# Kernel optimization log

Hardware: AMD Instinct MI355X
Metric: run time of the kernel (lower is better)

The kernel has to match this reference:

```python
import jax, jax.numpy as jnp
import numpy as np

BN_EPS = 1e-5
K = 3  # kernel size


def conv2d(x, w, b, pad):
    y = jax.lax.conv_general_dilated(
        x, w, window_strides=(1, 1), padding=[(pad, pad), (pad, pad)],
        dimension_numbers=('NCHW', 'OIHW', 'NCHW'))
    return y + b[None, :, None, None]


def setup_inputs() -> dict:
    key = jax.random.key(0)
    ks = jax.random.split(key, 4)
    B, C, H, W, O = 8, 256, 64, 64, 256
    x = jax.random.normal(ks[0], (B, C, H, W), dtype=jnp.float32)
    # offset/mask conv: 3*dg*k*k = 27 out channels; small init -> small offsets
    w_off = jax.random.normal(ks[1], (27, C, K, K), dtype=jnp.float32) * 0.01
    b_off = jnp.zeros((27,), dtype=jnp.float32)
    # main deformable conv weight/bias
    w = jax.random.normal(ks[2], (O, C, K, K), dtype=jnp.float32) * 0.05
    b = jnp.zeros((O,), dtype=jnp.float32)
    # BatchNorm (inference) params / running stats
    gamma = jnp.ones((O,), dtype=jnp.float32)
    beta = jnp.zeros((O,), dtype=jnp.float32)
    run_mean = jnp.zeros((O,), dtype=jnp.float32)
    run_var = jnp.ones((O,), dtype=jnp.float32)
    return {"x": x, "w_off": w_off, "b_off": b_off, "w": w, "b": b,
            "gamma": gamma, "beta": beta, "run_mean": run_mean, "run_var": run_var}


def _dcn_bn_relu(x, w_off, b_off, w, b, gamma, beta, run_mean, run_var):
    B, C, H, W = x.shape
    KK = K * K
    # offset + modulation mask (DCNv2): channels [0:9]=dy, [9:18]=dx, [18:27]=mask
    om = conv2d(x, w_off, b_off, pad=1)            # [B, 27, H, W]
    dy, dx = om[:, :KK], om[:, KK:2 * KK]          # [B, 9, H, W]
    mod = jax.nn.sigmoid(om[:, 2 * KK:])           # [B, 9, H, W]

    ky, kx = jnp.meshgrid(jnp.arange(K), jnp.arange(K), indexing='ij')
    # base sampling grid: out pixel + dilation*(k - center), padding=1
    base_y = jnp.arange(H, dtype=jnp.float32)[None, :, None] - 1.0 + ky.reshape(KK, 1, 1)
    base_x = jnp.arange(W, dtype=jnp.float32)[None, None, :] - 1.0 + kx.reshape(KK, 1, 1)
    py = base_y[None] + dy                          # [B, 9, H, W]
    px = base_x[None] + dx

    y0 = jnp.floor(py); x0 = jnp.floor(px)
    fy = py - y0; fx = px - x0
    y0 = y0.astype(jnp.int32); x0 = x0.astype(jnp.int32)

    x_flat = x.reshape(B, C, H * W)
    gather = jax.vmap(lambda xf, idx: xf[:, idx])   # ([C,HW],[9,H,W]) -> [C,9,H,W]

    def corner(yi, xi, wgt):
        valid = (yi >= 0) & (yi < H) & (xi >= 0) & (xi < W)
        idx = jnp.clip(yi, 0, H - 1) * W + jnp.clip(xi, 0, W - 1)
        val = gather(x_flat, idx)                   # [B, C, 9, H, W]
        return val * (wgt * valid.astype(wgt.dtype))[:, None]

    sampled = (corner(y0,     x0,     (1 - fy) * (1 - fx))
               + corner(y0,     x0 + 1, (1 - fy) * fx)
               + corner(y0 + 1, x0,     fy * (1 - fx))
               + corner(y0 + 1, x0 + 1, fy * fx))    # [B, C, 9, H, W]
    sampled = sampled * mod[:, None]                 # modulation

    O = w.shape[0]
    out = jnp.einsum('bckhw,ock->bohw', sampled, w.reshape(O, C, KK))
    out = out + b[None, :, None, None]

    # BatchNorm2d (inference) + ReLU
    inv = gamma / jnp.sqrt(run_var + BN_EPS)
    out = out * inv[None, :, None, None] + (beta - run_mean * inv)[None, :, None, None]
    return jax.nn.relu(out)


def reference(x, w_off, b_off, w, b, gamma, beta, run_mean, run_var):
    return _dcn_bn_relu(x, w_off, b_off, w, b, gamma, beta, run_mean, run_var)
```

## Files before the change

### kernel.cpp

```cpp
#include <hip/hip_runtime.h>
#include <math.h>

#define B_   8
#define C_   256
#define H_   64
#define W_   64
#define O_   256
#define KK_  9
#define CK_  2304
#define HW_  4096
#define BN_EPS 1e-5f

typedef __bf16 bf16x8 __attribute__((ext_vector_type(8)));
typedef float  f32x4  __attribute__((ext_vector_type(4)));

static __device__ __forceinline__ unsigned short f2bf(float f) {
    unsigned int u = __float_as_uint(f);
    unsigned int r = (u + 0x7fffu + ((u >> 16) & 1u)) >> 16;
    return (unsigned short)r;
}
static __device__ __forceinline__ unsigned int packbf2(float lo, float hi) {
    unsigned int ul = __float_as_uint(lo) + 0x8000u;
    unsigned int uh = __float_as_uint(hi) + 0x8000u;
    return __builtin_amdgcn_perm(uh, ul, 0x07060302u);
}
static __device__ __forceinline__ float bflo(unsigned int u) {
    return __uint_as_float(u << 16);
}
static __device__ __forceinline__ float bfhi(unsigned int u) {
    return __uint_as_float(u & 0xffff0000u);
}

__global__ __launch_bounds__(256) void prep_kernel(
    const float* __restrict__ x, const float* __restrict__ w,
    const float* __restrict__ w_off,
    unsigned short* __restrict__ xT, unsigned short* __restrict__ wKf,
    unsigned short* __restrict__ wof)
{
    __shared__ float tile[64][65];
    __shared__ float wbuf[4608];

    const int blk = blockIdx.x;
    const int tid = threadIdx.x, lane = tid & 63, tg = tid >> 6;

    if (blk < 512) {
        const int L = (blk & 7) * 64 + (blk >> 3);
        const int b = L & 7, h = L >> 3;
        const int hwb = h * W_;
#pragma unroll
        for (int ct = 0; ct < 4; ++ct) {
            const int c0 = ct * 64;
#pragma unroll
            for (int r = 0; r < 16; ++r) {
                int c_l = tg + r * 4;
                tile[c_l][lane] = x[((size_t)(b * C_ + c0 + c_l)) * HW_ + hwb + lane];
            }
            __syncthreads();
#pragma unroll
            for (int it = 0; it < 4; ++it) {
                const int hw_l = tg * 16 + it * 4 + (lane >> 4);
                const int c_l4 = (lane & 15) * 4;
                float v0 = tile[c_l4 + 0][hw_l];
                float v1 = tile[c_l4 + 1][hw_l];
                float v2 = tile[c_l4 + 2][hw_l];
                float v3 = tile[c_l4 + 3][hw_l];
                uint2 pk;
                pk.x = packbf2(v0, v1);
                pk.y = packbf2(v2, v3);
                *(uint2*)&xT[((size_t)(b * HW_ + hwb + hw_l)) * C_ + c0 + c_l4] = pk;
            }
            __syncthreads();
        }
    } else if (blk < 640) {
        const int t2 = blk - 512;
        const int NT = t2 >> 3, cb = t2 & 7;
#pragma unroll
        for (int i = 0; i < 18; ++i) {
            int j = i * 256 + tid;
            int o_l = j / 288, rest = j - o_l * 288;
            wbuf[o_l * 288 + rest] = w[(size_t)(NT * 16 + o_l) * CK_ + cb * 288 + rest];
        }
        __syncthreads();
#pragma unroll
        for (int i = 0; i < 18; ++i) {
            int d = i * 256 + tid;
            int tap = d >> 9, r5 = d & 511;
            int ln = r5 >> 3, e = r5 & 7;
            int n16 = ln & 15, q = ln >> 4;
            float val = wbuf[n16 * 288 + (q * 8 + e) * 9 + tap];
            wKf[((size_t)(NT * 72 + tap * 8 + cb) * 64 + ln) * 8 + e] = f2bf(val);
        }
    } else {
        const int t2 = blk - 640;
        const int NT = t2 >> 3, cb = t2 & 7;
#pragma unroll
        for (int i = 0; i < 18; ++i) {
            int j = i * 256 + tid;
            int o_l = j / 288, rest = j - o_l * 288;
            int o = NT * 16 + o_l;
            wbuf[o_l * 288 + rest] =
                (o < 27) ? w_off[(size_t)o * CK_ + cb * 288 + rest] : 0.f;
        }
        __syncthreads();
#pragma unroll
        for (int i = 0; i < 18; ++i) {
            int d = i * 256 + tid;
            int tap = d >> 9, r5 = d & 511;
            int ln = r5 >> 3, e = r5 & 7;
            int n16 = ln & 15, q = ln >> 4;
            float val = wbuf[n16 * 288 + (q * 8 + e) * 9 + tap];
            wof[((size_t)(NT * 72 + tap * 8 + cb) * 64 + ln) * 8 + e] = f2bf(val);
        }
    }
}

__global__ __launch_bounds__(512, 4) void dcn_fused_kernel(
    const unsigned short* __restrict__ xT, const unsigned short* __restrict__ wKf,
    const unsigned short* __restrict__ wof, const float* __restrict__ b_off,
    const float* __restrict__ bias, const float* __restrict__ gamma,
    const float* __restrict__ beta, const float* __restrict__ rmean,
    const float* __restrict__ rvar, float* __restrict__ out)
{
    __shared__ __align__(16) unsigned char smem[74528];
    unsigned short* rowbuf = (unsigned short*)smem;
    float4*         wgtv   = (float4*)smem;
    int4*           idxv   = (int4*)(smem + 9216);
    typedef float OmbT[27][64];
    OmbT& omb = *(OmbT*)(smem + 34848);
    typedef unsigned short AbufT[8][4][64][8];
    AbufT& Abuf = *(AbufT*)(smem + 41760);

    const int pblk = blockIdx.x;
    const int L = (pblk & 7) * 64 + (pblk >> 3);
    const int b = L & 7, h = L >> 3;
    const int tid = threadIdx.x, lane = tid & 63, wv = tid >> 6;
    const int m16 = lane & 15, q = lane >> 4;

    if (tid < 33) {
        *(uint4*)&rowbuf[tid * 8] = make_uint4(0u, 0u, 0u, 0u);
    } else if (tid >= 256 && tid < 289) {
        *(uint4*)&rowbuf[65 * 264 + (tid - 256) * 8] = make_uint4(0u, 0u, 0u, 0u);
    }

    const int mi_a = wv & 3, nj_a = wv >> 2;
    f32x4 oacc = {0.f, 0.f, 0.f, 0.f};
    const uint4* wof4 = (const uint4*)wof;

    for (int r = 0; r < 3; ++r) {
        const int hh = h - 1 + r;
        const bool vr = (hh >= 0) && (hh < H_);
        __syncthreads();
        if (vr) {
            const uint4* src = (const uint4*)&xT[((size_t)(b * HW_ + hh * W_)) * C_];
#pragma unroll
            for (int i = 0; i < 4; ++i) {
                const int idx8 = i * 512 + tid;
                uint4 v = src[idx8];
                const int px = idx8 >> 5, c8 = (idx8 & 31) * 8;
                *(uint4*)&rowbuf[(px + 1) * 264 + c8] = v;
            }
        }
        __syncthreads();
        if (vr) {
#pragma unroll
            for (int s = 0; s < 3; ++s) {
                const unsigned short* arow = &rowbuf[(mi_a * 16 + m16 + s) * 264 + q * 8];
#pragma unroll
                for (int cc = 0; cc < 8; ++cc) {
                    bf16x8 a = *(const bf16x8*)&arow[cc * 32];
                    uint4 braw = wof4[(size_t)(nj_a * 72 + (r * 3 + s) * 8 + cc) * 64 + lane];
                    oacc = __builtin_amdgcn_mfma_f32_16x16x32_bf16(
                        a, __builtin_bit_cast(bf16x8, braw), oacc, 0, 0, 0);
                }
            }
        }
    }
    {
        const int t = nj_a * 16 + m16;
        if (t < 27) {
            const float bo = b_off[t];
            float s0 = oacc[0] + bo, s1 = oacc[1] + bo,
                  s2 = oacc[2] + bo, s3 = oacc[3] + bo;
            if (t >= 18) {
                s0 = 1.f / (1.f + expf(-s0));
                s1 = 1.f / (1.f + expf(-s1));
                s2 = 1.f / (1.f + expf(-s2));
                s3 = 1.f / (1.f + expf(-s3));
            }
            float4 rr; rr.x = s0; rr.y = s1; rr.z = s2; rr.w = s3;
            *(float4*)&omb[t][mi_a * 16 + q * 4] = rr;
        }
    }
    __syncthreads();

    for (int i = tid; i < 576; i += 512) {
        int p = i / 9, t = i - p * 9;
        float dy = omb[t][p];
        float dx = omb[t + 9][p];
        float md = omb[t + 18][p];
        float py = (float)(h - 1 + t / 3) + dy;
        float px = (float)(p - 1 + t % 3) + dx;
        float y0f = floorf(py), x0f = floorf(px);
        int   y0 = (int)y0f,    x0 = (int)x0f;
        float fy = py - y0f,    fx = px - x0f;
        int y0c = min(max(y0,     0), H_ - 1), y1c = min(max(y0 + 1, 0), H_ - 1);
        int x0c = min(max(x0,     0), W_ - 1), x1c = min(max(x0 + 1, 0), W_ - 1);
        float vy0 = (y0     >= 0 && y0     < H_) ? 1.f : 0.f;
        float vy1 = (y0 + 1 >= 0 && y0 + 1 < H_) ? 1.f : 0.f;
        float vx0 = (x0     >= 0 && x0     < W_) ? 1.f : 0.f;
        float vx1 = (x0 + 1 >= 0 && x0 + 1 < W_) ? 1.f : 0.f;
        wgtv[i] = make_float4((1.f - fy) * (1.f - fx) * vy0 * vx0 * md,
                              (1.f - fy) * fx         * vy0 * vx1 * md,
                              fy         * (1.f - fx) * vy1 * vx0 * md,
                              fy         * fx         * vy1 * vx1 * md);
        const int rowb = (b * HW_) * (C_ * 2);
        idxv[i] = make_int4(rowb + (y0c * W_ + x0c) * (C_ * 2),
                            rowb + (y0c * W_ + x1c) * (C_ * 2),
                            rowb + (y1c * W_ + x0c) * (C_ * 2),
                            rowb + (y1c * W_ + x1c) * (C_ * 2));
    }
    __syncthreads();

    f32x4 acc[4][2];
#pragma unroll
    for (int mi = 0; mi < 4; ++mi)
#pragma unroll
        for (int nj = 0; nj < 2; ++nj)
#pragma unroll
            for (int r = 0; r < 4; ++r) acc[mi][nj][r] = 0.f;

    const uint4* wKf4 = (const uint4*)wKf;
    const char*  xTb  = (const char*)xT;

    const int s_cc = lane >> 3;
    const int s_q2 = (lane >> 1) & 3;
    const int s_j0 = (lane & 1) * 4;
    const int s_xr = (s_q2 << 1) ^ s_cc;
    const int s_mi = wv >> 1;
    const int s_pb = (wv & 1) * 8;
    const int loff = lane * 8;

    const int r_row = lane ^ ((lane >> 4) << 1);

    uint4 bA[4], bB[4];
    auto loadB = [&](uint4* dst, int t_, int p_) {
#pragma unroll
        for (int c2 = 0; c2 < 2; ++c2)
#pragma unroll
            for (int nj = 0; nj < 2; ++nj)
                dst[c2 * 2 + nj] =
                    wKf4[(size_t)((wv * 2 + nj) * 72 + t_ * 8 + p_ * 2 + c2) * 64 + lane];
    };
    auto mfmaPair = [&](int p_, const uint4* Bf) {
#pragma unroll
        for (int c2 = 0; c2 < 2; ++c2) {
            const int cc = p_ * 2 + c2;
            const int rr = r_row ^ cc;
            bf16x8 a[4];
#pragma unroll
            for (int mi = 0; mi < 4; ++mi)
                a[mi] = *(const bf16x8*)&Abuf[cc][mi][rr][0];
#pragma unroll
            for (int nj = 0; nj < 2; ++nj) {
                bf16x8 bb = __builtin_bit_cast(bf16x8, Bf[c2 * 2 + nj]);
#pragma unroll
                for (int mi = 0; mi < 4; ++mi)
                    acc[mi][nj] = __builtin_amdgcn_mfma_f32_16x16x32_bf16(
                        a[mi], bb, acc[mi][nj], 0, 0, 0);
            }
        }
    };

    loadB(bA, 0, 0);

#pragma unroll 1
    for (int tap = 0; tap < 9; ++tap) {
        uint2 pk[8];
#pragma unroll
        for (int pp = 0; pp < 8; ++pp) {
            const int p = wv * 8 + pp;
            const int4   iq = idxv[p * 9 + tap];
            const float4 wq = wgtv[p * 9 + tap];
            const uint2 k0 = *(const uint2*)(xTb + iq.x + loff);
            const uint2 k1 = *(const uint2*)(xTb + iq.y + loff);
            const uint2 k2 = *(const uint2*)(xTb + iq.z + loff);
            const uint2 k3 = *(const uint2*)(xTb + iq.w + loff);
            float g0 = wq.x*bflo(k0.x) + wq.y*bflo(k1.x) + wq.z*bflo(k2.x) + wq.w*bflo(k3.x);
            float g1 = wq.x*bfhi(k0.x) + wq.y*bfhi(k1.x) + wq.z*bfhi(k2.x) + wq.w*bfhi(k3.x);
            float g2 = wq.x*bflo(k0.y) + wq.y*bflo(k1.y) + wq.z*bflo(k2.y) + wq.w*bflo(k3.y);
            float g3 = wq.x*bfhi(k0.y) + wq.y*bfhi(k1.y) + wq.z*bfhi(k2.y) + wq.w*bfhi(k3.y);
            pk[pp].x = packbf2(g0, g1);
            pk[pp].y = packbf2(g2, g3);
        }

        __syncthreads();
#pragma unroll
        for (int pp = 0; pp < 8; ++pp) {
            const int P   = s_pb + pp;
            const int row = (P ^ s_xr) | (s_q2 << 4);
            *(uint2*)&Abuf[s_cc][s_mi][row][s_j0] = pk[pp];
        }
        __syncthreads();

        __builtin_amdgcn_s_setprio(1);
        loadB(bB, tap, 1);
        mfmaPair(0, bA);
        loadB(bA, tap, 2);
        mfmaPair(1, bB);
        loadB(bB, tap, 3);
        mfmaPair(2, bA);
        if (tap < 8) loadB(bA, tap + 1, 0);
        mfmaPair(3, bB);
        __builtin_amdgcn_s_setprio(0);
    }

#pragma unroll
    for (int nj = 0; nj < 2; ++nj) {
        const int o = wv * 32 + nj * 16 + (lane & 15);
        const float inv = gamma[o] * rsqrtf(rvar[o] + BN_EPS);
        const float sh  = beta[o] + (bias[o] - rmean[o]) * inv;
        float* ob = out + ((size_t)(b * O_ + o)) * HW_ + h * W_;
#pragma unroll
        for (int mi = 0; mi < 4; ++mi) {
            f32x4 v = acc[mi][nj];
            f32x4 r;
            r[0] = fmaxf(v[0] * inv + sh, 0.f);
            r[1] = fmaxf(v[1] * inv + sh, 0.f);
            r[2] = fmaxf(v[2] * inv + sh, 0.f);
            r[3] = fmaxf(v[3] * inv + sh, 0.f);
            __builtin_nontemporal_store(r, (f32x4*)&ob[mi * 16 + (lane >> 4) * 4]);
        }
    }
}

extern "C" void kernel_launch(void* const* d_in, const int* in_sizes, int n_in,
                              void* d_out, int out_size, void* d_ws, size_t ws_size,
                              hipStream_t stream) {
    const float* x     = (const float*)d_in[0];
    const float* w_off = (const float*)d_in[1];
    const float* b_off = (const float*)d_in[2];
    const float* w     = (const float*)d_in[3];
    const float* bias  = (const float*)d_in[4];
    const float* gamma = (const float*)d_in[5];
    const float* beta  = (const float*)d_in[6];
    const float* rmean = (const float*)d_in[7];
    const float* rvar  = (const float*)d_in[8];
    float* out = (float*)d_out;

    unsigned short* xT  = (unsigned short*)d_ws;
    unsigned short* wKf = xT + 8388608;
    unsigned short* wof = wKf + 589824;

    prep_kernel<<<656, 256, 0, stream>>>(x, w, w_off, xT, wKf, wof);
    dcn_fused_kernel<<<512, 512, 0, stream>>>(
        xT, wKf, wof, b_off, bias, gamma, beta, rmean, rvar, out);
}
```

Measured before the change: 177.9 us.

## Process two output rows per block to reuse weight loads

Each block now computes two output rows (128 pixels) instead of one, which halves the grid to 256 blocks. The offset conv streams four input rows and keeps its weight fragments in registers to feed both rows. The main GEMM reuses each B weight fragment across 8 M-tiles, so weight traffic per output is halved. Gather indices are packed into 16-bit pixel offsets to save shared memory. In exchange the kernel uses more registers and LDS, the launch bound drops to 2 blocks per CU, and 256 blocks may underfill the GPU's CUs.

Measured after the change: 199.2 us. 12.0% more time.

```diff
diff --git a/kernel.cpp b/kernel.cpp
--- a/kernel.cpp
+++ b/kernel.cpp
@@ -114,25 +114,26 @@
     }
 }
 
-__global__ __launch_bounds__(512, 4) void dcn_fused_kernel(
+__global__ __launch_bounds__(512, 2) void dcn_fused_kernel(
     const unsigned short* __restrict__ xT, const unsigned short* __restrict__ wKf,
     const unsigned short* __restrict__ wof, const float* __restrict__ b_off,
     const float* __restrict__ bias, const float* __restrict__ gamma,
     const float* __restrict__ beta, const float* __restrict__ rmean,
     const float* __restrict__ rvar, float* __restrict__ out)
 {
-    __shared__ __align__(16) unsigned char smem[74528];
+    __shared__ __align__(16) unsigned char smem[100384];
     unsigned short* rowbuf = (unsigned short*)smem;
-    float4*         wgtv   = (float4*)smem;
-    int4*           idxv   = (int4*)(smem + 9216);
-    typedef float OmbT[27][64];
+    float4*  wgtv = (float4*)smem;
+    ushort4* idxv = (ushort4*)(smem + 18432);
+    typedef float OmbT[27][128];
     OmbT& omb = *(OmbT*)(smem + 34848);
-    typedef unsigned short AbufT[8][4][64][8];
-    AbufT& Abuf = *(AbufT*)(smem + 41760);
+    typedef unsigned short AbufT[8][8][64][8];
+    AbufT& Abuf = *(AbufT*)(smem + 34848);
 
     const int pblk = blockIdx.x;
-    const int L = (pblk & 7) * 64 + (pblk >> 3);
-    const int b = L & 7, h = L >> 3;
+    const int L = (pblk & 7) * 32 + (pblk >> 3);
+    const int b = L & 7, hp = L >> 3;
+    const int h = hp * 2;
     const int tid = threadIdx.x, lane = tid & 63, wv = tid >> 6;
     const int m16 = lane & 15, q = lane >> 4;
 
@@ -143,11 +144,14 @@
     }
 
     const int mi_a = wv & 3, nj_a = wv >> 2;
-    f32x4 oacc = {0.f, 0.f, 0.f, 0.f};
+    f32x4 oacc0 = {0.f, 0.f, 0.f, 0.f};
+    f32x4 oacc1 = {0.f, 0.f, 0.f, 0.f};
     const uint4* wof4 = (const uint4*)wof;
-
-    for (int r = 0; r < 3; ++r) {
-        const int hh = h - 1 + r;
+    uint4 bsv[24];
+
+#pragma unroll
+    for (int st = 0; st < 4; ++st) {
+        const int hh = h - 1 + st;
         const bool vr = (hh >= 0) && (hh < H_);
         __syncthreads();
         if (vr) {
@@ -161,45 +165,57 @@
             }
         }
         __syncthreads();
-        if (vr) {
-#pragma unroll
-            for (int s = 0; s < 3; ++s) {
-                const unsigned short* arow = &rowbuf[(mi_a * 16 + m16 + s) * 264 + q * 8];
-#pragma unroll
-                for (int cc = 0; cc < 8; ++cc) {
-                    bf16x8 a = *(const bf16x8*)&arow[cc * 32];
-                    uint4 braw = wof4[(size_t)(nj_a * 72 + (r * 3 + s) * 8 + cc) * 64 + lane];
-                    oacc = __builtin_amdgcn_mfma_f32_16x16x32_bf16(
-                        a, __builtin_bit_cast(bf16x8, braw), oacc, 0, 0, 0);
+#pragma unroll
+        for (int s = 0; s < 3; ++s) {
+            const unsigned short* arow = &rowbuf[(mi_a * 16 + m16 + s) * 264 + q * 8];
+#pragma unroll
+            for (int cc = 0; cc < 8; ++cc) {
+                bf16x8 a;
+                if (vr) a = *(const bf16x8*)&arow[cc * 32];
+                if (st >= 1 && vr)
+                    oacc1 = __builtin_amdgcn_mfma_f32_16x16x32_bf16(
+                        a, __builtin_bit_cast(bf16x8, bsv[s * 8 + cc]), oacc1, 0, 0, 0);
+                if (st <= 2) {
+                    bsv[s * 8 + cc] =
+                        wof4[(size_t)(nj_a * 72 + (st * 3 + s) * 8 + cc) * 64 + lane];
+                    if (vr)
+                        oacc0 = __builtin_amdgcn_mfma_f32_16x16x32_bf16(
+                            a, __builtin_bit_cast(bf16x8, bsv[s * 8 + cc]), oacc0, 0, 0, 0);
                 }
             }
         }
     }
+    __syncthreads();
+
     {
         const int t = nj_a * 16 + m16;
         if (t < 27) {
             const float bo = b_off[t];
-            float s0 = oacc[0] + bo, s1 = oacc[1] + bo,
-                  s2 = oacc[2] + bo, s3 = oacc[3] + bo;
-            if (t >= 18) {
-                s0 = 1.f / (1.f + expf(-s0));
-                s1 = 1.f / (1.f + expf(-s1));
-                s2 = 1.f / (1.f + expf(-s2));
-                s3 = 1.f / (1.f + expf(-s3));
-            }
-            float4 rr; rr.x = s0; rr.y = s1; rr.z = s2; rr.w = s3;
-            *(float4*)&omb[t][mi_a * 16 + q * 4] = rr;
+#pragma unroll
+            for (int o = 0; o < 2; ++o) {
+                f32x4 v = o ? oacc1 : oacc0;
+                float s0 = v[0] + bo, s1 = v[1] + bo, s2 = v[2] + bo, s3 = v[3] + bo;
+                if (t >= 18) {
+                    s0 = 1.f / (1.f + expf(-s0));
+                    s1 = 1.f / (1.f + expf(-s1));
+                    s2 = 1.f / (1.f + expf(-s2));
+                    s3 = 1.f / (1.f + expf(-s3));
+                }
+                float4 rr; rr.x = s0; rr.y = s1; rr.z = s2; rr.w = s3;
+                *(float4*)&omb[t][o * 64 + mi_a * 16 + q * 4] = rr;
+            }
         }
     }
     __syncthreads();
 
-    for (int i = tid; i < 576; i += 512) {
+    for (int i = tid; i < 1152; i += 512) {
         int p = i / 9, t = i - p * 9;
+        int o = p >> 6, px_i = p & 63;
         float dy = omb[t][p];
         float dx = omb[t + 9][p];
         float md = omb[t + 18][p];
-        float py = (float)(h - 1 + t / 3) + dy;
-        float px = (float)(p - 1 + t % 3) + dx;
+        float py = (float)(h + o - 1 + t / 3) + dy;
+        float px = (float)(px_i - 1 + t % 3) + dx;
         float y0f = floorf(py), x0f = floorf(px);
         int   y0 = (int)y0f,    x0 = (int)x0f;
         float fy = py - y0f,    fx = px - x0f;
@@ -213,32 +229,30 @@
                               (1.f - fy) * fx         * vy0 * vx1 * md,
                               fy         * (1.f - fx) * vy1 * vx0 * md,
                               fy         * fx         * vy1 * vx1 * md);
-        const int rowb = (b * HW_) * (C_ * 2);
-        idxv[i] = make_int4(rowb + (y0c * W_ + x0c) * (C_ * 2),
-                            rowb + (y0c * W_ + x1c) * (C_ * 2),
-                            rowb + (y1c * W_ + x0c) * (C_ * 2),
-                            rowb + (y1c * W_ + x1c) * (C_ * 2));
+        ushort4 uu;
+        uu.x = (unsigned short)(y0c * W_ + x0c);
+        uu.y = (unsigned short)(y0c * W_ + x1c);
+        uu.z = (unsigned short)(y1c * W_ + x0c);
+        uu.w = (unsigned short)(y1c * W_ + x1c);
+        idxv[i] = uu;
     }
     __syncthreads();
 
-    f32x4 acc[4][2];
-#pragma unroll
-    for (int mi = 0; mi < 4; ++mi)
+    f32x4 acc[8][2];
+#pragma unroll
+    for (int mi = 0; mi < 8; ++mi)
 #pragma unroll
         for (int nj = 0; nj < 2; ++nj)
 #pragma unroll
             for (int r = 0; r < 4; ++r) acc[mi][nj][r] = 0.f;
 
     const uint4* wKf4 = (const uint4*)wKf;
-    const char*  xTb  = (const char*)xT;
+    const char* xTbL = (const char*)xT + (size_t)(b * HW_) * (C_ * 2) + lane * 8;
 
     const int s_cc = lane >> 3;
     const int s_q2 = (lane >> 1) & 3;
     const int s_j0 = (lane & 1) * 4;
     const int s_xr = (s_q2 << 1) ^ s_cc;
-    const int s_mi = wv >> 1;
-    const int s_pb = (wv & 1) * 8;
-    const int loff = lane * 8;
 
     const int r_row = lane ^ ((lane >> 4) << 1);
 
@@ -256,15 +270,15 @@
         for (int c2 = 0; c2 < 2; ++c2) {
             const int cc = p_ * 2 + c2;
             const int rr = r_row ^ cc;
-            bf16x8 a[4];
-#pragma unroll
-            for (int mi = 0; mi < 4; ++mi)
+            bf16x8 a[8];
+#pragma unroll
+            for (int mi = 0; mi < 8; ++mi)
                 a[mi] = *(const bf16x8*)&Abuf[cc][mi][rr][0];
 #pragma unroll
             for (int nj = 0; nj < 2; ++nj) {
                 bf16x8 bb = __builtin_bit_cast(bf16x8, Bf[c2 * 2 + nj]);
 #pragma unroll
-                for (int mi = 0; mi < 4; ++mi)
+                for (int mi = 0; mi < 8; ++mi)
                     acc[mi][nj] = __builtin_amdgcn_mfma_f32_16x16x32_bf16(
                         a[mi], bb, acc[mi][nj], 0, 0, 0);
             }
@@ -275,16 +289,16 @@
 
 #pragma unroll 1
     for (int tap = 0; tap < 9; ++tap) {
-        uint2 pk[8];
-#pragma unroll
-        for (int pp = 0; pp < 8; ++pp) {
-            const int p = wv * 8 + pp;
-            const int4   iq = idxv[p * 9 + tap];
-            const float4 wq = wgtv[p * 9 + tap];
-            const uint2 k0 = *(const uint2*)(xTb + iq.x + loff);
-            const uint2 k1 = *(const uint2*)(xTb + iq.y + loff);
-            const uint2 k2 = *(const uint2*)(xTb + iq.z + loff);
-            const uint2 k3 = *(const uint2*)(xTb + iq.w + loff);
+        uint2 pk[16];
+#pragma unroll
+        for (int pp = 0; pp < 16; ++pp) {
+            const int p = wv * 16 + pp;
+            const ushort4 iq = idxv[p * 9 + tap];
+            const float4  wq = wgtv[p * 9 + tap];
+            const uint2 k0 = *(const uint2*)(xTbL + ((int)iq.x << 9));
+            const uint2 k1 = *(const uint2*)(xTbL + ((int)iq.y << 9));
+            const uint2 k2 = *(const uint2*)(xTbL + ((int)iq.z << 9));
+            const uint2 k3 = *(const uint2*)(xTbL + ((int)iq.w << 9));
             float g0 = wq.x*bflo(k0.x) + wq.y*bflo(k1.x) + wq.z*bflo(k2.x) + wq.w*bflo(k3.x);
             float g1 = wq.x*bfhi(k0.x) + wq.y*bfhi(k1.x) + wq.z*bfhi(k2.x) + wq.w*bfhi(k3.x);
             float g2 = wq.x*bflo(k0.y) + wq.y*bflo(k1.y) + wq.z*bflo(k2.y) + wq.w*bflo(k3.y);
@@ -295,10 +309,9 @@
 
         __syncthreads();
 #pragma unroll
-        for (int pp = 0; pp < 8; ++pp) {
-            const int P   = s_pb + pp;
-            const int row = (P ^ s_xr) | (s_q2 << 4);
-            *(uint2*)&Abuf[s_cc][s_mi][row][s_j0] = pk[pp];
+        for (int pp = 0; pp < 16; ++pp) {
+            const int row = (pp ^ s_xr) | (s_q2 << 4);
+            *(uint2*)&Abuf[s_cc][wv][row][s_j0] = pk[pp];
         }
         __syncthreads();
 
@@ -316,19 +329,20 @@
 
 #pragma unroll
     for (int nj = 0; nj < 2; ++nj) {
-        const int o = wv * 32 + nj * 16 + (lane & 15);
+        const int o = wv * 32 + nj * 16 + m16;
         const float inv = gamma[o] * rsqrtf(rvar[o] + BN_EPS);
         const float sh  = beta[o] + (bias[o] - rmean[o]) * inv;
         float* ob = out + ((size_t)(b * O_ + o)) * HW_ + h * W_;
 #pragma unroll
-        for (int mi = 0; mi < 4; ++mi) {
+        for (int mi = 0; mi < 8; ++mi) {
             f32x4 v = acc[mi][nj];
             f32x4 r;
             r[0] = fmaxf(v[0] * inv + sh, 0.f);
             r[1] = fmaxf(v[1] * inv + sh, 0.f);
             r[2] = fmaxf(v[2] * inv + sh, 0.f);
             r[3] = fmaxf(v[3] * inv + sh, 0.f);
-            __builtin_nontemporal_store(r, (f32x4*)&ob[mi * 16 + (lane >> 4) * 4]);
+            __builtin_nontemporal_store(
+                r, (f32x4*)&ob[(mi >> 2) * W_ + (mi & 3) * 16 + q * 4]);
         }
     }
 }
@@ -352,6 +366,6 @@
     unsigned short* wof = wKf + 589824;
 
     prep_kernel<<<656, 256, 0, stream>>>(x, w, w_off, xT, wKf, wof);
-    dcn_fused_kernel<<<512, 512, 0, stream>>>(
+    dcn_fused_kernel<<<256, 512, 0, stream>>>(
         xT, wKf, wof, b_off, bias, gamma, beta, rmean, rvar, out);
 }
```
